# Performance work log

Hardware: AMD Instinct MI355X
Metric: run time of the kernel (lower is better)

## Reference

```python
import jax, jax.numpy as jnp
import numpy as np


def setup_inputs() -> dict:
    key = jax.random.key(0)
    k1, k2, k3, k4 = jax.random.split(key, 4)
    M, K, N = 16384, 1024, 4096
    # int8-range values stored as int32 (A8W8 path; int32 accumulation is identical)
    x = jax.random.randint(k1, (M, K), -128, 128, dtype=jnp.int32)
    weight = jax.random.randint(k2, (N, K), -128, 128, dtype=jnp.int32)
    scale = jax.random.uniform(k3, (N,), dtype=jnp.float32, minval=0.001, maxval=0.01)
    bias = jax.random.randint(k4, (N,), -64, 64, dtype=jnp.int32)
    return {"x": x, "weight": weight, "scale": scale, "bias": bias}


def reference(x, weight, scale, bias):
    # npu_quant_matmul: int32-accumulated matmul of quantized input with
    # weight^T, int32 bias add, then fused per-out-channel dequant scale.
    acc = jnp.matmul(x, weight.T) + bias[None, :]  # [M, N] int32
    return acc.astype(jnp.float32) * scale[None, :]  # dequantized output
```

## Files before the change

### kernel.cpp

```cpp
#include <hip/hip_runtime.h>

typedef __attribute__((ext_vector_type(4))) int int4v;

__global__ __launch_bounds__(256) void pack_i8_kernel(
    const int* __restrict__ src, int* __restrict__ dst, int n4)
{
    int i = blockIdx.x * blockDim.x + threadIdx.x;
    const int stride = gridDim.x * blockDim.x;
    for (; i < n4; i += stride) {
        int4v v = ((const int4v*)src)[i];
        int p = (v.x & 255) | ((v.y & 255) << 8) | ((v.z & 255) << 16) | ((v.w & 255) << 24);
        dst[i] = p;
    }
}

__global__ __launch_bounds__(256) void gemm_i8_kernel(
    const char* __restrict__ A8,
    const char* __restrict__ B8,
    const float* __restrict__ scale,
    const int* __restrict__ bias,
    float* __restrict__ out,
    int M, int N, int K)
{
    __shared__ __attribute__((aligned(16))) char lsA[128 * 128];
    __shared__ __attribute__((aligned(16))) char lsB[128 * 128];

    const int tid  = threadIdx.x;
    const int lane = tid & 63;
    const int wid  = tid >> 6;

    const int m0 = blockIdx.y * 128;
    const int n0 = blockIdx.x * 128;

    const int wr = wid >> 1, wc = wid & 1;
    const int wm0 = wr * 64, wn0 = wc * 64;

    const int r8 = lane >> 3;
    const int c8 = lane & 7;
    const int swzcol = ((c8 ^ r8) << 4);
    const int stRow = wid * 32;

    int4v acc[4][4];
#pragma unroll
    for (int i = 0; i < 4; ++i)
#pragma unroll
        for (int j = 0; j < 4; ++j)
            acc[i][j] = (int4v){0, 0, 0, 0};

    const int nkt = K >> 7;
    for (int t = 0; t < nkt; ++t) {
        const int k0 = t << 7;
#pragma unroll
        for (int j = 0; j < 4; ++j) {
            const char* srcA = A8 + (size_t)(m0 + stRow + j * 8 + r8) * K + (k0 + swzcol);
            const char* srcB = B8 + (size_t)(n0 + stRow + j * 8 + r8) * K + (k0 + swzcol);
            __builtin_amdgcn_global_load_lds(
                (const __attribute__((address_space(1))) void*)srcA,
                (__attribute__((address_space(3))) void*)(lsA + (stRow + j * 8) * 128),
                16, 0, 0);
            __builtin_amdgcn_global_load_lds(
                (const __attribute__((address_space(1))) void*)srcB,
                (__attribute__((address_space(3))) void*)(lsB + (stRow + j * 8) * 128),
                16, 0, 0);
        }
        __syncthreads();

#pragma unroll
        for (int kk = 0; kk < 2; ++kk) {
            int4v af[4], bf[4];
#pragma unroll
            for (int i = 0; i < 4; ++i) {
                const int rowA = wm0 + i * 16 + (lane & 15);
                const int col  = (kk * 64 + (lane >> 4) * 16) ^ ((rowA & 7) << 4);
                af[i] = *(const int4v*)(lsA + rowA * 128 + col);
                const int rowB = wn0 + i * 16 + (lane & 15);
                bf[i] = *(const int4v*)(lsB + rowB * 128 + col);
            }
#pragma unroll
            for (int i = 0; i < 4; ++i)
#pragma unroll
                for (int j = 0; j < 4; ++j)
                    acc[i][j] = __builtin_amdgcn_mfma_i32_16x16x64_i8(af[i], bf[j], acc[i][j], 0, 0, 0);
        }
        __syncthreads();
    }

    const int lc = lane & 15;
    const int lq = lane >> 4;
    float scl[4];
    int   bsv[4];
#pragma unroll
    for (int j = 0; j < 4; ++j) {
        const int col = n0 + wn0 + j * 16 + lc;
        scl[j] = scale[col];
        bsv[j] = bias[col];
    }
#pragma unroll
    for (int i = 0; i < 4; ++i) {
        const int rowb = m0 + wm0 + i * 16 + lq * 4;
#pragma unroll
        for (int j = 0; j < 4; ++j) {
            const int col = n0 + wn0 + j * 16 + lc;
#pragma unroll
            for (int r = 0; r < 4; ++r) {
                out[(size_t)(rowb + r) * N + col] = (float)(acc[i][j][r] + bsv[j]) * scl[j];
            }
        }
    }
}

__global__ __launch_bounds__(256) void naive_kernel(
    const int* __restrict__ x, const int* __restrict__ w,
    const float* __restrict__ scale, const int* __restrict__ bias,
    float* __restrict__ out, int M, int N, int K)
{
    size_t idx = (size_t)blockIdx.x * blockDim.x + threadIdx.x;
    const size_t total = (size_t)M * N;
    const size_t stride = (size_t)gridDim.x * blockDim.x;
    for (; idx < total; idx += stride) {
        const int m = (int)(idx / N), n = (int)(idx % N);
        int acc = 0;
        for (int k = 0; k < K; ++k) acc += x[(size_t)m * K + k] * w[(size_t)n * K + k];
        out[idx] = (float)(acc + bias[n]) * scale[n];
    }
}

extern "C" void kernel_launch(void* const* d_in, const int* in_sizes, int n_in,
                              void* d_out, int out_size, void* d_ws, size_t ws_size,
                              hipStream_t stream)
{
    const int*   x     = (const int*)d_in[0];
    const int*   w     = (const int*)d_in[1];
    const float* scale = (const float*)d_in[2];
    const int*   bias  = (const int*)d_in[3];
    float*       out   = (float*)d_out;

    const int N = in_sizes[2];
    const int K = in_sizes[1] / N;
    const int M = in_sizes[0] / K;

    const size_t needA = (size_t)M * K;
    const size_t needB = (size_t)N * K;

    if (ws_size < needA + needB || (M % 128) || (N % 128) || (K % 128)) {
        const int blocks = 8192;
        naive_kernel<<<blocks, 256, 0, stream>>>(x, w, scale, bias, out, M, N, K);
        return;
    }

    char* x8 = (char*)d_ws;
    char* w8 = x8 + needA;

    pack_i8_kernel<<<4096, 256, 0, stream>>>(x, (int*)x8, (M * K) >> 2);
    pack_i8_kernel<<<4096, 256, 0, stream>>>(w, (int*)w8, (N * K) >> 2);

    dim3 grid(N / 128, M / 128);
    gemm_i8_kernel<<<grid, 256, 0, stream>>>(x8, w8, scale, bias, out, M, N, K);
}
```

Baseline: 128.9 us.

## Rewrite int8 GEMM as 256x256 double-buffered pipelined kernel with XCD remap

Replaces the 128x128 single-buffered GEMM with a 256x256 tile, 512-thread kernel that double-buffers K-tiles in 128KB of dynamic LDS. Global-to-LDS loads for the next tile are interleaved with MFMA phases, using explicit barriers, waitcnts and setprio. Workgroup IDs are remapped across 8 chiplets (XCDs) to improve L2 locality, and the two pack kernels are merged into one launch. This aims to hide load latency and raise arithmetic intensity, at the cost of more registers, much more LDS per block, and a fragile hand-written sync schedule.

```diff
diff --git a/kernel.cpp b/kernel.cpp
--- a/kernel.cpp
+++ b/kernel.cpp
@@ -2,109 +2,194 @@
 
 typedef __attribute__((ext_vector_type(4))) int int4v;
 
-__global__ __launch_bounds__(256) void pack_i8_kernel(
-    const int* __restrict__ src, int* __restrict__ dst, int n4)
+#define AS1 __attribute__((address_space(1)))
+#define AS3 __attribute__((address_space(3)))
+
+#define BAR()   __builtin_amdgcn_s_barrier()
+#define LGKM0() asm volatile("s_waitcnt lgkmcnt(0)" ::: "memory")
+
+#define STG_A(sb, rowbase, k0) \
+    __builtin_amdgcn_global_load_lds( \
+        (const AS1 void*)(aSrcBase + (size_t)(rowbase) * K + (k0)), \
+        (AS3 void*)(ldsDestA + (sb) + (rowbase) * 128), 16, 0, 0)
+#define STG_B(sb, rowbase, k0) \
+    __builtin_amdgcn_global_load_lds( \
+        (const AS1 void*)(bSrcBase + (size_t)(rowbase) * K + (k0)), \
+        (AS3 void*)(ldsDestB + (sb) + (rowbase) * 128), 16, 0, 0)
+
+#define LDA(mq, sb) \
+    { _Pragma("unroll") for (int m = 0; m < 4; ++m) { \
+        const int rb = (sb) + ((aRow0 + ((mq) << 6) + (m << 4)) << 7); \
+        a[m][0] = *(const int4v*)(ls + rb + colx0); \
+        a[m][1] = *(const int4v*)(ls + rb + colx1); } }
+
+#define LDB(nq, sb) \
+    { _Pragma("unroll") for (int n = 0; n < 2; ++n) { \
+        const int rb = (sb) + 32768 + ((bRow0 + ((nq) << 5) + (n << 4)) << 7); \
+        b[(nq)*2 + n][0] = *(const int4v*)(ls + rb + colx0); \
+        b[(nq)*2 + n][1] = *(const int4v*)(ls + rb + colx1); } }
+
+#define MMA(mq, nq) \
+    { __builtin_amdgcn_s_setprio(1); \
+      _Pragma("unroll") for (int m = 0; m < 4; ++m) \
+      _Pragma("unroll") for (int n = 0; n < 2; ++n) { \
+        acc[(mq)*4 + m][(nq)*2 + n] = __builtin_amdgcn_mfma_i32_16x16x64_i8( \
+            a[m][0], b[(nq)*2 + n][0], acc[(mq)*4 + m][(nq)*2 + n], 0, 0, 0); \
+        acc[(mq)*4 + m][(nq)*2 + n] = __builtin_amdgcn_mfma_i32_16x16x64_i8( \
+            a[m][1], b[(nq)*2 + n][1], acc[(mq)*4 + m][(nq)*2 + n], 0, 0, 0); } \
+      __builtin_amdgcn_s_setprio(0); }
+
+__global__ __launch_bounds__(256) void pack_both_kernel(
+    const int* __restrict__ x, const int* __restrict__ w,
+    int* __restrict__ x8, int* __restrict__ w8, int n4x, int n4w)
 {
     int i = blockIdx.x * blockDim.x + threadIdx.x;
     const int stride = gridDim.x * blockDim.x;
-    for (; i < n4; i += stride) {
-        int4v v = ((const int4v*)src)[i];
-        int p = (v.x & 255) | ((v.y & 255) << 8) | ((v.z & 255) << 16) | ((v.w & 255) << 24);
-        dst[i] = p;
-    }
-}
-
-__global__ __launch_bounds__(256) void gemm_i8_kernel(
-    const char* __restrict__ A8,
-    const char* __restrict__ B8,
-    const float* __restrict__ scale,
-    const int* __restrict__ bias,
-    float* __restrict__ out,
-    int M, int N, int K)
-{
-    __shared__ __attribute__((aligned(16))) char lsA[128 * 128];
-    __shared__ __attribute__((aligned(16))) char lsB[128 * 128];
+    const int tot = n4x + n4w;
+    for (; i < tot; i += stride) {
+        const bool isx = i < n4x;
+        const int4v v = isx ? ((const int4v*)x)[i] : ((const int4v*)w)[i - n4x];
+        const int p = (v.x & 255) | ((v.y & 255) << 8) | ((v.z & 255) << 16) | ((v.w & 255) << 24);
+        if (isx) x8[i] = p; else w8[i - n4x] = p;
+    }
+}
+
+__global__ __launch_bounds__(512, 2) void gemm_i8_256(
+    const char* __restrict__ A8, const char* __restrict__ B8,
+    const float* __restrict__ scale, const int* __restrict__ bias,
+    float* __restrict__ out, int M, int N, int K, int nwg_n)
+{
+    extern __shared__ __attribute__((aligned(16))) char ls[];
 
     const int tid  = threadIdx.x;
     const int lane = tid & 63;
     const int wid  = tid >> 6;
-
-    const int m0 = blockIdx.y * 128;
-    const int n0 = blockIdx.x * 128;
-
-    const int wr = wid >> 1, wc = wid & 1;
-    const int wm0 = wr * 64, wn0 = wc * 64;
-
-    const int r8 = lane >> 3;
-    const int c8 = lane & 7;
-    const int swzcol = ((c8 ^ r8) << 4);
-    const int stRow = wid * 32;
-
-    int4v acc[4][4];
-#pragma unroll
-    for (int i = 0; i < 4; ++i)
+    const int wr   = wid >> 2;
+    const int wc   = wid & 3;
+    const int l15  = lane & 15;
+    const int hi16 = lane >> 4;
+
+    int wg = blockIdx.x;
+    {
+        const int nwg = gridDim.x;
+        const int q = nwg >> 3, r = nwg & 7;
+        const int x = wg & 7, lq = wg >> 3;
+        wg = (x < r ? x * (q + 1) : r * (q + 1) + (x - r) * q) + lq;
+    }
+    const int m0 = (wg / nwg_n) << 8;
+    const int n0 = (wg % nwg_n) << 8;
+
+    const int sw    = (l15 & 7) << 4;
+    const int colx0 = ((hi16 << 4)) ^ sw;
+    const int colx1 = (64 + (hi16 << 4)) ^ sw;
+    const int aRow0 = (wr << 7) + l15;
+    const int bRow0 = (wc << 6) + l15;
+
+    const int srow  = tid >> 3;
+    const int sslot = tid & 7;
+    const int scol  = ((sslot ^ (srow & 7)) << 4);
+    const char* aSrcBase = A8 + (size_t)(m0 + srow) * K + scol;
+    const char* bSrcBase = B8 + (size_t)(n0 + srow) * K + scol;
+    char* ldsDestA = ls + srow * 128 + (sslot << 4);
+    char* ldsDestB = ls + 32768 + srow * 128 + (sslot << 4);
+
+    int4v acc[8][4];
+#pragma unroll
+    for (int i = 0; i < 8; ++i)
 #pragma unroll
         for (int j = 0; j < 4; ++j)
             acc[i][j] = (int4v){0, 0, 0, 0};
 
+    int4v a[4][2], b[4][2];
+
     const int nkt = K >> 7;
-    for (int t = 0; t < nkt; ++t) {
-        const int k0 = t << 7;
-#pragma unroll
-        for (int j = 0; j < 4; ++j) {
-            const char* srcA = A8 + (size_t)(m0 + stRow + j * 8 + r8) * K + (k0 + swzcol);
-            const char* srcB = B8 + (size_t)(n0 + stRow + j * 8 + r8) * K + (k0 + swzcol);
-            __builtin_amdgcn_global_load_lds(
-                (const __attribute__((address_space(1))) void*)srcA,
-                (__attribute__((address_space(3))) void*)(lsA + (stRow + j * 8) * 128),
-                16, 0, 0);
-            __builtin_amdgcn_global_load_lds(
-                (const __attribute__((address_space(1))) void*)srcB,
-                (__attribute__((address_space(3))) void*)(lsB + (stRow + j * 8) * 128),
-                16, 0, 0);
-        }
-        __syncthreads();
-
-#pragma unroll
-        for (int kk = 0; kk < 2; ++kk) {
-            int4v af[4], bf[4];
-#pragma unroll
-            for (int i = 0; i < 4; ++i) {
-                const int rowA = wm0 + i * 16 + (lane & 15);
-                const int col  = (kk * 64 + (lane >> 4) * 16) ^ ((rowA & 7) << 4);
-                af[i] = *(const int4v*)(lsA + rowA * 128 + col);
-                const int rowB = wn0 + i * 16 + (lane & 15);
-                bf[i] = *(const int4v*)(lsB + rowB * 128 + col);
-            }
-#pragma unroll
-            for (int i = 0; i < 4; ++i)
-#pragma unroll
-                for (int j = 0; j < 4; ++j)
-                    acc[i][j] = __builtin_amdgcn_mfma_i32_16x16x64_i8(af[i], bf[j], acc[i][j], 0, 0, 0);
-        }
-        __syncthreads();
-    }
-
-    const int lc = lane & 15;
-    const int lq = lane >> 4;
-    float scl[4];
-    int   bsv[4];
-#pragma unroll
-    for (int j = 0; j < 4; ++j) {
-        const int col = n0 + wn0 + j * 16 + lc;
-        scl[j] = scale[col];
-        bsv[j] = bias[col];
-    }
-#pragma unroll
-    for (int i = 0; i < 4; ++i) {
-        const int rowb = m0 + wm0 + i * 16 + lq * 4;
-#pragma unroll
-        for (int j = 0; j < 4; ++j) {
-            const int col = n0 + wn0 + j * 16 + lc;
-#pragma unroll
-            for (int r = 0; r < 4; ++r) {
-                out[(size_t)(rowb + r) * N + col] = (float)(acc[i][j][r] + bsv[j]) * scl[j];
-            }
+    const int nit = nkt >> 1;
+
+    STG_A(0, 0, 0);   STG_A(0, 128, 0);
+    STG_A(0, 64, 0);  STG_A(0, 192, 0);
+    STG_B(0, 0, 0);   STG_B(0, 64, 0);
+    STG_B(0, 128, 0); STG_B(0, 192, 0);
+    STG_A(65536, 0, 128); STG_A(65536, 128, 128);
+    STG_B(65536, 0, 128); STG_B(65536, 64, 128);
+    STG_B(65536, 128, 128); STG_B(65536, 192, 128);
+    asm volatile("s_waitcnt vmcnt(6)" ::: "memory");
+    BAR();
+
+#pragma unroll 1
+    for (int it = 0; it < nit; ++it) {
+        const int kO1 = (2 * it + 1) << 7;
+        const int tE = 2 * it + 2, tO = 2 * it + 3;
+        const int kE = tE << 7, kO = tO << 7;
+        const bool ok = tE < nkt;
+
+        LDA(0, 0); LDB(0, 0);
+        STG_A(65536, 64, kO1); STG_A(65536, 192, kO1);
+        BAR(); LGKM0();
+        MMA(0, 0);
+        BAR();
+
+        LDB(1, 0);
+        if (ok) { STG_A(0, 0, kE); STG_A(0, 128, kE); }
+        BAR(); LGKM0();
+        MMA(0, 1);
+        BAR();
+
+        LDA(1, 0);
+        if (ok) { STG_B(0, 0, kE); STG_B(0, 64, kE); }
+        BAR(); LGKM0();
+        MMA(1, 1);
+        BAR();
+
+        if (ok) { STG_B(0, 128, kE); STG_B(0, 192, kE); }
+        BAR(); LGKM0();
+        MMA(1, 0);
+        if (ok) { asm volatile("s_waitcnt vmcnt(6)" ::: "memory"); }
+        else    { asm volatile("s_waitcnt vmcnt(0)" ::: "memory"); }
+        BAR();
+
+        LDA(0, 65536); LDB(0, 65536);
+        if (ok) { STG_A(0, 64, kE); STG_A(0, 192, kE); }
+        BAR(); LGKM0();
+        MMA(0, 0);
+        BAR();
+
+        LDB(1, 65536);
+        if (ok) { STG_A(65536, 0, kO); STG_A(65536, 128, kO); }
+        BAR(); LGKM0();
+        MMA(0, 1);
+        BAR();
+
+        LDA(1, 65536);
+        if (ok) { STG_B(65536, 0, kO); STG_B(65536, 64, kO); }
+        BAR(); LGKM0();
+        MMA(1, 1);
+        BAR();
+
+        if (ok) { STG_B(65536, 128, kO); STG_B(65536, 192, kO); }
+        BAR(); LGKM0();
+        MMA(1, 0);
+        if (ok) { asm volatile("s_waitcnt vmcnt(6)" ::: "memory"); }
+        else    { asm volatile("s_waitcnt vmcnt(0)" ::: "memory"); }
+        BAR();
+    }
+
+    float scl[4]; int bsv[4];
+#pragma unroll
+    for (int nj = 0; nj < 4; ++nj) {
+        const int col = n0 + (wc << 6) + (nj << 4) + l15;
+        scl[nj] = scale[col];
+        bsv[nj] = bias[col];
+    }
+#pragma unroll
+    for (int mi = 0; mi < 8; ++mi) {
+        const int rowb = m0 + (wr << 7) + (mi << 4) + (hi16 << 2);
+#pragma unroll
+        for (int nj = 0; nj < 4; ++nj) {
+            const int col = n0 + (wc << 6) + (nj << 4) + l15;
+            float* o = out + (size_t)rowb * N + col;
+#pragma unroll
+            for (int r = 0; r < 4; ++r)
+                o[(size_t)r * N] = (float)(acc[mi][nj][r] + bsv[nj]) * scl[nj];
         }
     }
 }
@@ -142,18 +227,21 @@
     const size_t needA = (size_t)M * K;
     const size_t needB = (size_t)N * K;
 
-    if (ws_size < needA + needB || (M % 128) || (N % 128) || (K % 128)) {
-        const int blocks = 8192;
-        naive_kernel<<<blocks, 256, 0, stream>>>(x, w, scale, bias, out, M, N, K);
+    if (ws_size < needA + needB || (M % 256) || (N % 256) || (K % 256)) {
+        naive_kernel<<<8192, 256, 0, stream>>>(x, w, scale, bias, out, M, N, K);
         return;
     }
 
     char* x8 = (char*)d_ws;
     char* w8 = x8 + needA;
 
-    pack_i8_kernel<<<4096, 256, 0, stream>>>(x, (int*)x8, (M * K) >> 2);
-    pack_i8_kernel<<<4096, 256, 0, stream>>>(w, (int*)w8, (N * K) >> 2);
-
-    dim3 grid(N / 128, M / 128);
-    gemm_i8_kernel<<<grid, 256, 0, stream>>>(x8, w8, scale, bias, out, M, N, K);
-}
+    pack_both_kernel<<<2048, 256, 0, stream>>>(x, w, (int*)x8, (int*)w8,
+                                               (int)(needA >> 2), (int)(needB >> 2));
+
+    hipFuncSetAttribute((const void*)gemm_i8_256,
+                        hipFuncAttributeMaxDynamicSharedMemorySize, 131072);
+
+    const int nwg_n = N / 256;
+    const int nwg = (M / 256) * nwg_n;
+    gemm_i8_256<<<nwg, 512, 131072, stream>>>(x8, w8, scale, bias, out, M, N, K, nwg_n);
+}
```

Result: no change. 127.9 us (-0.8%).
